# Optimization experiments

Hardware: AMD Instinct MI355X
Metric: run time of the kernel (lower is better)

## Reference

```python
import jax, jax.numpy as jnp
import numpy as np

N_NODES_PER_GRAPH = 64
NUM_GRAPHS = 2048
N = NUM_GRAPHS * N_NODES_PER_GRAPH  # 131072 total nodes
E = N * 8                           # 1048576 edges
IN_DIM, H1, H2 = 64, 128, 64
OUT_DIM = (N_NODES_PER_GRAPH * N_NODES_PER_GRAPH - N_NODES_PER_GRAPH) // 2  # 2016


def setup_inputs() -> dict:
    key = jax.random.key(0)
    ks = jax.random.split(key, 16)
    s = 0.05
    x = jax.random.normal(ks[0], (N, IN_DIM), dtype=jnp.float32)
    # edges within each graph: offsets within graph + graph base offset
    src_local = jax.random.randint(ks[1], (E,), 0, N_NODES_PER_GRAPH)
    dst_local = jax.random.randint(ks[2], (E,), 0, N_NODES_PER_GRAPH)
    gid = jnp.repeat(jnp.arange(NUM_GRAPHS), E // NUM_GRAPHS) * N_NODES_PER_GRAPH
    edge_index = jnp.stack([src_local + gid, dst_local + gid]).astype(jnp.int64)
    batch = jnp.repeat(jnp.arange(NUM_GRAPHS), N_NODES_PER_GRAPH).astype(jnp.int64)
    eps = jax.random.normal(ks[3], (NUM_GRAPHS, H2), dtype=jnp.float32)
    return {
        "x": x, "edge_index": edge_index, "batch": batch, "eps": eps,
        "w1_rel": jax.random.normal(ks[4], (IN_DIM, H1)) * s,
        "b1": jnp.zeros((H1,), jnp.float32),
        "w1_root": jax.random.normal(ks[5], (IN_DIM, H1)) * s,
        "w2_rel": jax.random.normal(ks[6], (H1, H2)) * s,
        "b2": jnp.zeros((H2,), jnp.float32),
        "w2_root": jax.random.normal(ks[7], (H1, H2)) * s,
        "w3_rel": jax.random.normal(ks[8], (H1, H2)) * s,
        "b3": jnp.zeros((H2,), jnp.float32),
        "w3_root": jax.random.normal(ks[9], (H1, H2)) * s,
        "fc1_w": jax.random.normal(ks[10], (H2, H1)) * s,
        "fc1_b": jnp.zeros((H1,), jnp.float32),
        "fc2_w": jax.random.normal(ks[11], (H1, OUT_DIM)) * s,
        "fc2_b": jnp.zeros((OUT_DIM,), jnp.float32),
    }


def _graph_conv(h, src, dst, w_rel, b, w_root):
    # PyG GraphConv: out_i = W_rel @ (sum_{j in N(i)} h_j) + b + W_root @ h_i
    agg = jax.ops.segment_sum(h[src], dst, num_segments=N)  # [N, d_in]
    return agg @ w_rel + b + h @ w_root


def _segment_mean(h, seg):
    s = jax.ops.segment_sum(h, seg, num_segments=NUM_GRAPHS)
    cnt = jax.ops.segment_sum(jnp.ones((h.shape[0],), h.dtype), seg, num_segments=NUM_GRAPHS)
    return s / jnp.maximum(cnt, 1.0)[:, None]


def reference(x, edge_index, batch, eps, w1_rel, b1, w1_root, w2_rel, b2, w2_root,
              w3_rel, b3, w3_root, fc1_w, fc1_b, fc2_w, fc2_b):
    src, dst = edge_index[0], edge_index[1]
    # encode (dropout p=0.0 -> identity)
    h1 = jax.nn.relu(_graph_conv(x, src, dst, w1_rel, b1, w1_root))
    mu = _segment_mean(_graph_conv(h1, src, dst, w2_rel, b2, w2_root), batch)
    logvar = _segment_mean(_graph_conv(h1, src, dst, w3_rel, b3, w3_root), batch)
    # reparameterize with provided eps
    z = mu + eps * jnp.exp(0.5 * logvar)
    # decode
    h = jax.nn.relu(z @ fc1_w + fc1_b)
    recon = jax.nn.sigmoid(h @ fc2_w + fc2_b)
    return recon, mu, logvar
```

## Files before the change

### kernel.cpp

```cpp
#include <hip/hip_runtime.h>
#include <math.h>

#define NG 2048
#define NPG 64
#define EPG 512
#define ETOT (NG*EPG)
#define IND 64
#define H1D 128
#define H2D 64
#define OUTD 2016

typedef __attribute__((ext_vector_type(8))) short bf16x8;
typedef __attribute__((ext_vector_type(4))) float f32x4;
typedef __attribute__((ext_vector_type(8))) unsigned short u16x8;
typedef __attribute__((ext_vector_type(4))) short s16x4;

__device__ inline short f2b(float f) {
  union { float f; unsigned u; } v; v.f = f;
  unsigned r = (v.u + 0x7FFFu + ((v.u >> 16) & 1u)) >> 16;
  return (short)r;
}

__global__ void p_w1(const float* __restrict__ w1_rel, const float* __restrict__ w1_root,
                     short* __restrict__ WTgF,
                     const float* __restrict__ w2_rel, const float* __restrict__ w2_root,
                     const float* __restrict__ w3_rel, const float* __restrict__ w3_root,
                     const float* __restrict__ fc1_w,
                     short* __restrict__ W23T, short* __restrict__ fc1T) {
  __shared__ float L[4224];
  const int b = blockIdx.x;
  const int tid = threadIdx.x;
  if (b < 8) {
    const int ct = b;
    const int ks = tid >> 6, l = tid & 63;
    const int col = ct*16 + (l & 15);
    const int kb  = ks*32 + (l >> 4)*8;
    short tmp[8];
    #pragma unroll
    for (int j = 0; j < 8; ++j) {
      const int k = kb + j;
      float v = (k < 64) ? w1_rel[k*H1D + col] : w1_root[(k - 64)*H1D + col];
      tmp[j] = f2b(v);
    }
    *(uint4*)&WTgF[(size_t)((ct*4 + ks)*64 + l)*8] = *(uint4*)tmp;
  } else if (b < 12) {
    const int cc = b - 8;
    const int j0 = cc*32;
    const float* wrel  = (cc < 2) ? w2_rel  : w3_rel;
    const float* wroot = (cc < 2) ? w2_root : w3_root;
    const int jl = j0 & 63;
    const int c = tid >> 3, k0 = (tid & 7)*32;
    for (int i = tid; i < 4096; i += 256) {
      int k = i >> 5, cc2 = i & 31;
      L[k*33 + cc2] = wrel[k*H2D + jl + cc2];
    }
    __syncthreads();
    if (k0 < 128)
      for (int kk = 0; kk < 32; ++kk)
        W23T[(size_t)(j0 + c)*264 + k0 + kk] = f2b(L[(k0 + kk)*33 + c]);
    __syncthreads();
    for (int i = tid; i < 4096; i += 256) {
      int k = i >> 5, cc2 = i & 31;
      L[k*33 + cc2] = wroot[k*H2D + jl + cc2];
    }
    __syncthreads();
    if (k0 >= 128)
      for (int kk = 0; kk < 32; ++kk)
        W23T[(size_t)(j0 + c)*264 + k0 + kk] = f2b(L[(k0 + kk - 128)*33 + c]);
  } else {
    const int c0 = (b - 12)*64;
    for (int i = tid; i < 4096; i += 256) {
      int k = i >> 6, c = i & 63;
      L[k*65 + c] = fc1_w[k*H1D + c0 + c];
    }
    __syncthreads();
    const int c = tid >> 2, k0 = (tid & 3)*16;
    for (int kk = 0; kk < 16; ++kk)
      fc1T[(size_t)(c0 + c)*72 + k0 + kk] = f2b(L[(k0 + kk)*65 + c]);
  }
}

__global__ __launch_bounds__(256, 5) void k1_enc(
    const float* __restrict__ x, const int* __restrict__ ei,
    const short* __restrict__ WTgF, const float* __restrict__ b1,
    short* __restrict__ SVb,
    const float* __restrict__ fc2_w, short* __restrict__ WF2g)
{
  __shared__ __align__(16) char smem[31744];
  const int g = blockIdx.x;
  const int tid = threadIdx.x;

  if (g >= NG) {
    float* L = (float*)smem;
    const int bid = g - NG;
    const int c0 = bid*32;
    for (int i = tid; i < 4096; i += 256) {
      int k = i >> 5, c = i & 31;
      L[k*33 + c] = fc2_w[(size_t)k*OUTD + c0 + c];
    }
    __syncthreads();
    const int tl = tid >> 7;
    const int r  = tid & 127;
    const int ks = r >> 5;
    const int lp = r & 31;
    const int ct = bid*2 + tl;
    #pragma unroll
    for (int u = 0; u < 2; ++u) {
      const int l = lp*2 + u;
      const int cl = tl*16 + (l & 15);
      const int kb = ks*32 + (l >> 4)*8;
      short tmp[8];
      #pragma unroll
      for (int j = 0; j < 8; ++j) tmp[j] = f2b(L[(kb + j)*33 + cl]);
      *(uint4*)&WF2g[(size_t)((ct*4 + ks)*64 + l)*8] = *(uint4*)tmp;
    }
    return;
  }

  short* Xb   = (short*)smem;
  short* XbT  = (short*)(smem + 9216);
  short* Ab   = (short*)(smem + 18432);
  unsigned* Au32 = (unsigned*)(smem + 27648);

  const int w = tid >> 6, l = tid & 63;

  const int e0 = g*EPG + tid*2;
  const int2 sp = *(const int2*)&ei[e0];
  const int2 dp = *(const int2*)&ei[ETOT + e0];
  const int s0 = sp.x & 63, d0 = dp.x & 63;
  const int s1 = sp.y & 63, d1 = dp.y & 63;
  const int n = tid >> 2, f0 = (tid & 3) * 16;
  const float* xr = x + (size_t)g*(NPG*IND) + n*IND + f0;
  float4 v0 = *(const float4*)&xr[0];
  float4 v1 = *(const float4*)&xr[4];
  float4 v2 = *(const float4*)&xr[8];
  float4 v3 = *(const float4*)&xr[12];

  for (int i = tid; i < 64*16; i += 256) Au32[i] = 0u;
  __syncthreads();

  atomicAdd(&Au32[d0*16 + (s0 >> 2)], 1u << (8*(s0 & 3)));
  atomicAdd(&Au32[d1*16 + (s1 >> 2)], 1u << (8*(s1 & 3)));

  {
    u16x8 lo, hi;
    lo[0]=(unsigned short)f2b(v0.x); lo[1]=(unsigned short)f2b(v0.y);
    lo[2]=(unsigned short)f2b(v0.z); lo[3]=(unsigned short)f2b(v0.w);
    lo[4]=(unsigned short)f2b(v1.x); lo[5]=(unsigned short)f2b(v1.y);
    lo[6]=(unsigned short)f2b(v1.z); lo[7]=(unsigned short)f2b(v1.w);
    hi[0]=(unsigned short)f2b(v2.x); hi[1]=(unsigned short)f2b(v2.y);
    hi[2]=(unsigned short)f2b(v2.z); hi[3]=(unsigned short)f2b(v2.w);
    hi[4]=(unsigned short)f2b(v3.x); hi[5]=(unsigned short)f2b(v3.y);
    hi[6]=(unsigned short)f2b(v3.z); hi[7]=(unsigned short)f2b(v3.w);
    *(u16x8*)&Xb[n*72 + f0]     = lo;
    *(u16x8*)&Xb[n*72 + f0 + 8] = hi;
    #pragma unroll
    for (int j = 0; j < 8; ++j) {
      XbT[(f0 + j)*72 + n]     = (short)lo[j];
      XbT[(f0 + 8 + j)*72 + n] = (short)hi[j];
    }
  }
  __syncthreads();

  {
    const int row = tid >> 2, qw = tid & 3;
    unsigned wds[4];
    #pragma unroll
    for (int q = 0; q < 4; ++q) wds[q] = Au32[row*16 + qw*4 + q];
    auto pk = [](unsigned wv, int p) -> unsigned {
      unsigned c0 = (wv >> (16*p)) & 255u, c1 = (wv >> (16*p + 8)) & 255u;
      return (unsigned)(unsigned short)f2b((float)c0)
           | ((unsigned)(unsigned short)f2b((float)c1) << 16);
    };
    uint4 oA = { pk(wds[0],0), pk(wds[0],1), pk(wds[1],0), pk(wds[1],1) };
    uint4 oB = { pk(wds[2],0), pk(wds[2],1), pk(wds[3],0), pk(wds[3],1) };
    unsigned* abp = (unsigned*)&Ab[row*72 + qw*16];
    *(uint4*)&abp[0] = oA;
    *(uint4*)&abp[4] = oB;
  }

  {
    const int squad = tid >> 4;
    const int db = (tid & 15) * 4;
    unsigned ps = 0;
    #pragma unroll
    for (int i = 0; i < 4; ++i) ps += Au32[(db + i)*16 + squad];
    ps += __shfl_xor(ps, 1); ps += __shfl_xor(ps, 2);
    ps += __shfl_xor(ps, 4); ps += __shfl_xor(ps, 8);
    if ((tid & 15) == 0) {
      #pragma unroll
      for (int i = 0; i < 4; ++i)
        *(float*)&Ab[(squad*4 + i)*72 + 64] = (float)((ps >> (8*i)) & 255u);
    }
  }

  const int rm = w*16;
  const int fr = l & 15;
  const int koff = (l >> 4) * 8;

  f32x4 agc[4];
  #pragma unroll
  for (int t = 0; t < 4; ++t) agc[t] = (f32x4){0.f,0.f,0.f,0.f};
  #pragma unroll
  for (int ks = 0; ks < 2; ++ks) {
    bf16x8 a = *(const bf16x8*)&Ab[(rm + fr)*72 + ks*32 + koff];
    #pragma unroll
    for (int t = 0; t < 4; ++t) {
      bf16x8 b = *(const bf16x8*)&XbT[(t*16 + fr)*72 + ks*32 + koff];
      agc[t] = __builtin_amdgcn_mfma_f32_16x16x32_bf16(a, b, agc[t], 0, 0, 0);
    }
  }

  bf16x8 bfr[2][4];
  #pragma unroll
  for (int ct2 = 0; ct2 < 2; ++ct2)
    #pragma unroll
    for (int ks = 0; ks < 4; ++ks)
      bfr[ct2][ks] = *(const bf16x8*)&WTgF[(size_t)(((2*w + ct2)*4 + ks)*64 + l)*8];

  short* AGb = Ab;
  #pragma unroll
  for (int t = 0; t < 4; ++t)
    #pragma unroll
    for (int r = 0; r < 4; ++r)
      AGb[(rm + (l>>4)*4 + r)*72 + t*16 + fr] = f2b(agc[t][r]);

  __syncthreads();

  const float bb0 = b1[(2*w)*16 + fr];
  const float bb1 = b1[(2*w + 1)*16 + fr];
  float hs0 = 0.f, ws0 = 0.f, hs1 = 0.f, ws1 = 0.f;
  #pragma unroll
  for (int rt = 0; rt < 4; ++rt) {
    bf16x8 afr[4];
    #pragma unroll
    for (int ks = 0; ks < 4; ++ks)
      afr[ks] = (ks < 2)
        ? *(const bf16x8*)&AGb[(rt*16 + fr)*72 + ks*32 + koff]
        : *(const bf16x8*)&Xb[(rt*16 + fr)*72 + (ks - 2)*32 + koff];
    f32x4 a0 = (f32x4){0.f,0.f,0.f,0.f}, a1 = (f32x4){0.f,0.f,0.f,0.f};
    #pragma unroll
    for (int ks = 0; ks < 4; ++ks) {
      a0 = __builtin_amdgcn_mfma_f32_16x16x32_bf16(afr[ks], bfr[0][ks], a0, 0, 0, 0);
      a1 = __builtin_amdgcn_mfma_f32_16x16x32_bf16(afr[ks], bfr[1][ks], a1, 0, 0, 0);
    }
    #pragma unroll
    for (int r = 0; r < 4; ++r) {
      const float dgr = *(const float*)&Ab[(rt*16 + (l>>4)*4 + r)*72 + 64];
      float va = fmaxf(a0[r] + bb0, 0.f);
      float vb = fmaxf(a1[r] + bb1, 0.f);
      hs0 += va; ws0 += dgr*va;
      hs1 += vb; ws1 += dgr*vb;
    }
  }
  hs0 += __shfl_down(hs0, 32); ws0 += __shfl_down(ws0, 32);
  hs1 += __shfl_down(hs1, 32); ws1 += __shfl_down(ws1, 32);
  hs0 += __shfl_down(hs0, 16); ws0 += __shfl_down(ws0, 16);
  hs1 += __shfl_down(hs1, 16); ws1 += __shfl_down(ws1, 16);
  if (l < 16) {
    short* svg = SVb + (size_t)g*256;
    svg[(2*w)*16 + l]           = f2b(ws0);
    svg[(2*w + 1)*16 + l]       = f2b(ws1);
    svg[128 + (2*w)*16 + l]     = f2b(hs0);
    svg[128 + (2*w + 1)*16 + l] = f2b(hs1);
  }
}

__global__ __launch_bounds__(256) void k1b_latent(
    const short* __restrict__ SVb, const short* __restrict__ W23T,
    const float* __restrict__ b2, const float* __restrict__ b3,
    const float* __restrict__ eps, const short* __restrict__ fc1T,
    const float* __restrict__ fc1_b,
    float* __restrict__ out_mu, float* __restrict__ out_lv, short* __restrict__ hbufF)
{
  __shared__ short SV[32*264];
  __shared__ short Zt[32*72];
  const int g0 = blockIdx.x * 32;
  const int tid = threadIdx.x;
  const int w = tid >> 6, l = tid & 63;
  const int s = w >> 1;
  const int h = w & 1;
  const int fr = l & 15;
  const int koff = (l >> 4) * 8;

  for (int i = tid; i < 32*64; i += 256) {
    const int r = i >> 6, kq = (i & 63)*4;
    *(s16x4*)&SV[r*264 + kq] = *(const s16x4*)&SVb[(size_t)(g0 + r)*256 + kq];
  }
  __syncthreads();

  f32x4 acc[4];
  #pragma unroll
  for (int t = 0; t < 4; ++t) acc[t] = (f32x4){0.f,0.f,0.f,0.f};
  #pragma unroll
  for (int ks = 0; ks < 8; ++ks) {
    bf16x8 a = *(const bf16x8*)&SV[(s*16 + fr)*264 + ks*32 + koff];
    #pragma unroll
    for (int j = 0; j < 2; ++j) {
      bf16x8 bm = *(const bf16x8*)&W23T[((2*h + j)*16 + fr)*264 + ks*32 + koff];
      bf16x8 bl = *(const bf16x8*)&W23T[((2*h + j + 4)*16 + fr)*264 + ks*32 + koff];
      acc[j]     = __builtin_amdgcn_mfma_f32_16x16x32_bf16(bm, a, acc[j], 0, 0, 0);
      acc[2 + j] = __builtin_amdgcn_mfma_f32_16x16x32_bf16(bl, a, acc[2 + j], 0, 0, 0);
    }
  }
  {
    const int grow = s*16 + (l & 15);
    const size_t gg = (size_t)(g0 + grow);
    #pragma unroll
    for (int j = 0; j < 2; ++j) {
      const int c0 = (2*h + j)*16 + (l >> 4)*4;
      const float4 bb2 = *(const float4*)&b2[c0];
      const float4 bb3 = *(const float4*)&b3[c0];
      const float4 ev  = *(const float4*)&eps[gg*64 + c0];
      float4 mu, lv;
      mu.x = acc[j][0]*(1.f/64.f) + bb2.x;  lv.x = acc[2+j][0]*(1.f/64.f) + bb3.x;
      mu.y = acc[j][1]*(1.f/64.f) + bb2.y;  lv.y = acc[2+j][1]*(1.f/64.f) + bb3.y;
      mu.z = acc[j][2]*(1.f/64.f) + bb2.z;  lv.z = acc[2+j][2]*(1.f/64.f) + bb3.z;
      mu.w = acc[j][3]*(1.f/64.f) + bb2.w;  lv.w = acc[2+j][3]*(1.f/64.f) + bb3.w;
      *(float4*)&out_mu[gg*64 + c0] = mu;
      *(float4*)&out_lv[gg*64 + c0] = lv;
      s16x4 zs;
      zs[0] = f2b(mu.x + ev.x * __expf(0.5f*lv.x));
      zs[1] = f2b(mu.y + ev.y * __expf(0.5f*lv.y));
      zs[2] = f2b(mu.z + ev.z * __expf(0.5f*lv.z));
      zs[3] = f2b(mu.w + ev.w * __expf(0.5f*lv.w));
      *(s16x4*)&Zt[grow*72 + c0] = zs;
    }
  }
  __syncthreads();

  f32x4 hacc[4];
  #pragma unroll
  for (int t = 0; t < 4; ++t) hacc[t] = (f32x4){0.f,0.f,0.f,0.f};
  #pragma unroll
  for (int ks = 0; ks < 2; ++ks) {
    bf16x8 a = *(const bf16x8*)&Zt[(s*16 + fr)*72 + ks*32 + koff];
    #pragma unroll
    for (int j = 0; j < 4; ++j) {
      bf16x8 b = *(const bf16x8*)&fc1T[((h*4 + j)*16 + fr)*72 + ks*32 + koff];
      hacc[j] = __builtin_amdgcn_mfma_f32_16x16x32_bf16(b, a, hacc[j], 0, 0, 0);
    }
  }
  {
    const int row = s*16 + (l & 15);
    const int rt2 = blockIdx.x*2 + (row >> 4);
    #pragma unroll
    for (int j = 0; j < 4; ++j) {
      const int c0 = (h*4 + j)*16 + (l >> 4)*4;
      const float4 bb = *(const float4*)&fc1_b[c0];
      s16x4 hv;
      hv[0] = f2b(fmaxf(hacc[j][0] + bb.x, 0.f));
      hv[1] = f2b(fmaxf(hacc[j][1] + bb.y, 0.f));
      hv[2] = f2b(fmaxf(hacc[j][2] + bb.z, 0.f));
      hv[3] = f2b(fmaxf(hacc[j][3] + bb.w, 0.f));
      const int ks2 = c0 >> 5;
      const int q   = (c0 >> 3) & 3;
      const int j8  = c0 & 7;
      const int lane = (row & 15) + 16*q;
      *(s16x4*)&hbufF[(size_t)((rt2*4 + ks2)*64 + lane)*8 + j8] = hv;
    }
  }
}

__global__ __launch_bounds__(256, 8) void k2_decoder(
    const short* __restrict__ hbufF, const short* __restrict__ WF2g,
    const float* __restrict__ fc2_b, float* __restrict__ recon)
{
  const int bx = blockIdx.x, by = blockIdx.y;
  const int tid = threadIdx.x;
  const int w = tid >> 6, l = tid & 63;
  const int rt = bx*4 + w;

  bf16x8 ah[4];
  #pragma unroll
  for (int ks = 0; ks < 4; ++ks)
    ah[ks] = *(const bf16x8*)&hbufF[(size_t)((rt*4 + ks)*64 + l)*8];

  f32x4 acc[6];
  #pragma unroll
  for (int t = 0; t < 6; ++t) acc[t] = (f32x4){0.f,0.f,0.f,0.f};

  #pragma unroll
  for (int ks = 0; ks < 4; ++ks) {
    #pragma unroll
    for (int t = 0; t < 6; ++t) {
      const int ct = by*6 + t;
      bf16x8 bw = *(const bf16x8*)&WF2g[(size_t)((ct*4 + ks)*64 + l)*8];
      acc[t] = __builtin_amdgcn_mfma_f32_16x16x32_bf16(bw, ah[ks], acc[t], 0, 0, 0);
    }
  }

  const int row = bx*64 + w*16 + (l & 15);
  #pragma unroll
  for (int t = 0; t < 6; ++t) {
    const int colq = (by*6 + t)*16 + (l >> 4)*4;
    const float4 bb = *(const float4*)&fc2_b[colq];
    float4 o;
    o.x = 1.f/(1.f + __expf(-(acc[t][0] + bb.x)));
    o.y = 1.f/(1.f + __expf(-(acc[t][1] + bb.y)));
    o.z = 1.f/(1.f + __expf(-(acc[t][2] + bb.z)));
    o.w = 1.f/(1.f + __expf(-(acc[t][3] + bb.w)));
    *(float4*)&recon[(size_t)row*OUTD + colq] = o;
  }
}

extern "C" void kernel_launch(void* const* d_in, const int* in_sizes, int n_in,
                              void* d_out, int out_size, void* d_ws, size_t ws_size,
                              hipStream_t stream) {
  const float* x       = (const float*)d_in[0];
  const int*   ei      = (const int*)d_in[1];
  const float* eps     = (const float*)d_in[3];
  const float* w1_rel  = (const float*)d_in[4];
  const float* b1      = (const float*)d_in[5];
  const float* w1_root = (const float*)d_in[6];
  const float* w2_rel  = (const float*)d_in[7];
  const float* b2      = (const float*)d_in[8];
  const float* w2_root = (const float*)d_in[9];
  const float* w3_rel  = (const float*)d_in[10];
  const float* b3      = (const float*)d_in[11];
  const float* w3_root = (const float*)d_in[12];
  const float* fc1_w   = (const float*)d_in[13];
  const float* fc1_b   = (const float*)d_in[14];
  const float* fc2_w   = (const float*)d_in[15];
  const float* fc2_b   = (const float*)d_in[16];

  float* recon  = (float*)d_out;
  float* out_mu = recon + (size_t)NG*OUTD;
  float* out_lv = out_mu + (size_t)NG*H2D;

  char* p = (char*)d_ws;
  short* WTgF  = (short*)p;              p += 8*4*64*8*2;
  short* WF2g  = (short*)p;              p += 126*4*64*8*2;
  short* fc1T  = (short*)p;              p += 128*72*2;
  short* W23T  = (short*)p;              p += 128*264*2;
  short* SVb   = (short*)p;              p += (size_t)NG*256*2;
  short* hbufF = (short*)p;

  p_w1<<<14, 256, 0, stream>>>(w1_rel, w1_root, WTgF,
                               w2_rel, w2_root, w3_rel, w3_root,
                               fc1_w, W23T, fc1T);
  k1_enc<<<NG + 63, 256, 0, stream>>>(x, ei, WTgF, b1, SVb, fc2_w, WF2g);
  k1b_latent<<<64, 256, 0, stream>>>(SVb, W23T, b2, b3, eps, fc1T, fc1_b,
                                     out_mu, out_lv, hbufF);
  k2_decoder<<<dim3(32, 21), 256, 0, stream>>>(hbufF, WF2g, fc2_b, recon);
}
```

Baseline: 135.2 us.

## Process two graphs per encoder block with prefetched second-graph loads

After: 140.5 us. +3.9%, slower.

```diff
diff --git a/kernel.cpp b/kernel.cpp
--- a/kernel.cpp
+++ b/kernel.cpp
@@ -80,19 +80,19 @@
   }
 }
 
-__global__ __launch_bounds__(256, 5) void k1_enc(
+__global__ __launch_bounds__(256, 4) void k1_enc(
     const float* __restrict__ x, const int* __restrict__ ei,
     const short* __restrict__ WTgF, const float* __restrict__ b1,
     short* __restrict__ SVb,
     const float* __restrict__ fc2_w, short* __restrict__ WF2g)
 {
-  __shared__ __align__(16) char smem[31744];
+  __shared__ __align__(16) char smem[35840];
   const int g = blockIdx.x;
   const int tid = threadIdx.x;
 
-  if (g >= NG) {
+  if (g >= NG/2) {
     float* L = (float*)smem;
-    const int bid = g - NG;
+    const int bid = g - NG/2;
     const int c0 = bid*32;
     for (int i = tid; i < 4096; i += 256) {
       int k = i >> 5, c = i & 31;
@@ -120,29 +120,29 @@
   short* Xb   = (short*)smem;
   short* XbT  = (short*)(smem + 9216);
   short* Ab   = (short*)(smem + 18432);
-  unsigned* Au32 = (unsigned*)(smem + 27648);
+  unsigned* AuA = (unsigned*)(smem + 27648);
+  unsigned* AuB = (unsigned*)(smem + 31744);
 
   const int w = tid >> 6, l = tid & 63;
-
-  const int e0 = g*EPG + tid*2;
-  const int2 sp = *(const int2*)&ei[e0];
-  const int2 dp = *(const int2*)&ei[ETOT + e0];
-  const int s0 = sp.x & 63, d0 = dp.x & 63;
-  const int s1 = sp.y & 63, d1 = dp.y & 63;
+  const int fr = l & 15;
+  const int koff = (l >> 4) * 8;
+  const int rm = w*16;
   const int n = tid >> 2, f0 = (tid & 3) * 16;
-  const float* xr = x + (size_t)g*(NPG*IND) + n*IND + f0;
-  float4 v0 = *(const float4*)&xr[0];
-  float4 v1 = *(const float4*)&xr[4];
-  float4 v2 = *(const float4*)&xr[8];
-  float4 v3 = *(const float4*)&xr[12];
-
-  for (int i = tid; i < 64*16; i += 256) Au32[i] = 0u;
-  __syncthreads();
-
-  atomicAdd(&Au32[d0*16 + (s0 >> 2)], 1u << (8*(s0 & 3)));
-  atomicAdd(&Au32[d1*16 + (s1 >> 2)], 1u << (8*(s1 & 3)));
-
-  {
+
+  const int gA = g*2;
+  const int e0 = gA*EPG + tid*2;
+  const int2 spA = *(const int2*)&ei[e0];
+  const int2 dpA = *(const int2*)&ei[ETOT + e0];
+  const int2 spB = *(const int2*)&ei[e0 + EPG];
+  const int2 dpB = *(const int2*)&ei[ETOT + e0 + EPG];
+
+  const float* xrA = x + (size_t)gA*(NPG*IND) + n*IND + f0;
+  float4 va0 = *(const float4*)&xrA[0];
+  float4 va1 = *(const float4*)&xrA[4];
+  float4 va2 = *(const float4*)&xrA[8];
+  float4 va3 = *(const float4*)&xrA[12];
+
+  auto STAGE = [&](float4 v0, float4 v1, float4 v2, float4 v3) {
     u16x8 lo, hi;
     lo[0]=(unsigned short)f2b(v0.x); lo[1]=(unsigned short)f2b(v0.y);
     lo[2]=(unsigned short)f2b(v0.z); lo[3]=(unsigned short)f2b(v0.w);
@@ -159,14 +159,13 @@
       XbT[(f0 + j)*72 + n]     = (short)lo[j];
       XbT[(f0 + 8 + j)*72 + n] = (short)hi[j];
     }
-  }
-  __syncthreads();
-
-  {
+  };
+
+  auto CVT = [&](const unsigned* Au) {
     const int row = tid >> 2, qw = tid & 3;
     unsigned wds[4];
     #pragma unroll
-    for (int q = 0; q < 4; ++q) wds[q] = Au32[row*16 + qw*4 + q];
+    for (int q = 0; q < 4; ++q) wds[q] = Au[row*16 + qw*4 + q];
     auto pk = [](unsigned wv, int p) -> unsigned {
       unsigned c0 = (wv >> (16*p)) & 255u, c1 = (wv >> (16*p + 8)) & 255u;
       return (unsigned)(unsigned short)f2b((float)c0)
@@ -177,14 +176,11 @@
     unsigned* abp = (unsigned*)&Ab[row*72 + qw*16];
     *(uint4*)&abp[0] = oA;
     *(uint4*)&abp[4] = oB;
-  }
-
-  {
     const int squad = tid >> 4;
     const int db = (tid & 15) * 4;
     unsigned ps = 0;
     #pragma unroll
-    for (int i = 0; i < 4; ++i) ps += Au32[(db + i)*16 + squad];
+    for (int i = 0; i < 4; ++i) ps += Au[(db + i)*16 + squad];
     ps += __shfl_xor(ps, 1); ps += __shfl_xor(ps, 2);
     ps += __shfl_xor(ps, 4); ps += __shfl_xor(ps, 8);
     if ((tid & 15) == 0) {
@@ -192,24 +188,27 @@
       for (int i = 0; i < 4; ++i)
         *(float*)&Ab[(squad*4 + i)*72 + 64] = (float)((ps >> (8*i)) & 255u);
     }
-  }
-
-  const int rm = w*16;
-  const int fr = l & 15;
-  const int koff = (l >> 4) * 8;
-
-  f32x4 agc[4];
-  #pragma unroll
-  for (int t = 0; t < 4; ++t) agc[t] = (f32x4){0.f,0.f,0.f,0.f};
-  #pragma unroll
-  for (int ks = 0; ks < 2; ++ks) {
-    bf16x8 a = *(const bf16x8*)&Ab[(rm + fr)*72 + ks*32 + koff];
-    #pragma unroll
-    for (int t = 0; t < 4; ++t) {
-      bf16x8 b = *(const bf16x8*)&XbT[(t*16 + fr)*72 + ks*32 + koff];
-      agc[t] = __builtin_amdgcn_mfma_f32_16x16x32_bf16(a, b, agc[t], 0, 0, 0);
-    }
-  }
+  };
+
+  auto PH1 = [&]() {
+    f32x4 agc[4];
+    #pragma unroll
+    for (int t = 0; t < 4; ++t) agc[t] = (f32x4){0.f,0.f,0.f,0.f};
+    #pragma unroll
+    for (int ks = 0; ks < 2; ++ks) {
+      bf16x8 a = *(const bf16x8*)&Ab[(rm + fr)*72 + ks*32 + koff];
+      #pragma unroll
+      for (int t = 0; t < 4; ++t) {
+        bf16x8 b = *(const bf16x8*)&XbT[(t*16 + fr)*72 + ks*32 + koff];
+        agc[t] = __builtin_amdgcn_mfma_f32_16x16x32_bf16(a, b, agc[t], 0, 0, 0);
+      }
+    }
+    #pragma unroll
+    for (int t = 0; t < 4; ++t)
+      #pragma unroll
+      for (int r = 0; r < 4; ++r)
+        Ab[(rm + (l>>4)*4 + r)*72 + t*16 + fr] = f2b(agc[t][r]);
+  };
 
   bf16x8 bfr[2][4];
   #pragma unroll
@@ -217,53 +216,75 @@
     #pragma unroll
     for (int ks = 0; ks < 4; ++ks)
       bfr[ct2][ks] = *(const bf16x8*)&WTgF[(size_t)(((2*w + ct2)*4 + ks)*64 + l)*8];
-
-  short* AGb = Ab;
-  #pragma unroll
-  for (int t = 0; t < 4; ++t)
-    #pragma unroll
-    for (int r = 0; r < 4; ++r)
-      AGb[(rm + (l>>4)*4 + r)*72 + t*16 + fr] = f2b(agc[t][r]);
-
-  __syncthreads();
-
   const float bb0 = b1[(2*w)*16 + fr];
   const float bb1 = b1[(2*w + 1)*16 + fr];
-  float hs0 = 0.f, ws0 = 0.f, hs1 = 0.f, ws1 = 0.f;
-  #pragma unroll
-  for (int rt = 0; rt < 4; ++rt) {
-    bf16x8 afr[4];
-    #pragma unroll
-    for (int ks = 0; ks < 4; ++ks)
-      afr[ks] = (ks < 2)
-        ? *(const bf16x8*)&AGb[(rt*16 + fr)*72 + ks*32 + koff]
-        : *(const bf16x8*)&Xb[(rt*16 + fr)*72 + (ks - 2)*32 + koff];
-    f32x4 a0 = (f32x4){0.f,0.f,0.f,0.f}, a1 = (f32x4){0.f,0.f,0.f,0.f};
-    #pragma unroll
-    for (int ks = 0; ks < 4; ++ks) {
-      a0 = __builtin_amdgcn_mfma_f32_16x16x32_bf16(afr[ks], bfr[0][ks], a0, 0, 0, 0);
-      a1 = __builtin_amdgcn_mfma_f32_16x16x32_bf16(afr[ks], bfr[1][ks], a1, 0, 0, 0);
-    }
-    #pragma unroll
-    for (int r = 0; r < 4; ++r) {
-      const float dgr = *(const float*)&Ab[(rt*16 + (l>>4)*4 + r)*72 + 64];
-      float va = fmaxf(a0[r] + bb0, 0.f);
-      float vb = fmaxf(a1[r] + bb1, 0.f);
-      hs0 += va; ws0 += dgr*va;
-      hs1 += vb; ws1 += dgr*vb;
-    }
-  }
-  hs0 += __shfl_down(hs0, 32); ws0 += __shfl_down(ws0, 32);
-  hs1 += __shfl_down(hs1, 32); ws1 += __shfl_down(ws1, 32);
-  hs0 += __shfl_down(hs0, 16); ws0 += __shfl_down(ws0, 16);
-  hs1 += __shfl_down(hs1, 16); ws1 += __shfl_down(ws1, 16);
-  if (l < 16) {
-    short* svg = SVb + (size_t)g*256;
-    svg[(2*w)*16 + l]           = f2b(ws0);
-    svg[(2*w + 1)*16 + l]       = f2b(ws1);
-    svg[128 + (2*w)*16 + l]     = f2b(hs0);
-    svg[128 + (2*w + 1)*16 + l] = f2b(hs1);
-  }
+
+  auto PH2EPI = [&](int gg) {
+    float hs0 = 0.f, ws0 = 0.f, hs1 = 0.f, ws1 = 0.f;
+    #pragma unroll
+    for (int rt = 0; rt < 4; ++rt) {
+      bf16x8 afr[4];
+      #pragma unroll
+      for (int ks = 0; ks < 4; ++ks)
+        afr[ks] = (ks < 2)
+          ? *(const bf16x8*)&Ab[(rt*16 + fr)*72 + ks*32 + koff]
+          : *(const bf16x8*)&Xb[(rt*16 + fr)*72 + (ks - 2)*32 + koff];
+      f32x4 a0 = (f32x4){0.f,0.f,0.f,0.f}, a1 = (f32x4){0.f,0.f,0.f,0.f};
+      #pragma unroll
+      for (int ks = 0; ks < 4; ++ks) {
+        a0 = __builtin_amdgcn_mfma_f32_16x16x32_bf16(afr[ks], bfr[0][ks], a0, 0, 0, 0);
+        a1 = __builtin_amdgcn_mfma_f32_16x16x32_bf16(afr[ks], bfr[1][ks], a1, 0, 0, 0);
+      }
+      #pragma unroll
+      for (int r = 0; r < 4; ++r) {
+        const float dgr = *(const float*)&Ab[(rt*16 + (l>>4)*4 + r)*72 + 64];
+        float va = fmaxf(a0[r] + bb0, 0.f);
+        float vb = fmaxf(a1[r] + bb1, 0.f);
+        hs0 += va; ws0 += dgr*va;
+        hs1 += vb; ws1 += dgr*vb;
+      }
+    }
+    hs0 += __shfl_down(hs0, 32); ws0 += __shfl_down(ws0, 32);
+    hs1 += __shfl_down(hs1, 32); ws1 += __shfl_down(ws1, 32);
+    hs0 += __shfl_down(hs0, 16); ws0 += __shfl_down(ws0, 16);
+    hs1 += __shfl_down(hs1, 16); ws1 += __shfl_down(ws1, 16);
+    if (l < 16) {
+      short* svg = SVb + (size_t)gg*256;
+      svg[(2*w)*16 + l]           = f2b(ws0);
+      svg[(2*w + 1)*16 + l]       = f2b(ws1);
+      svg[128 + (2*w)*16 + l]     = f2b(hs0);
+      svg[128 + (2*w + 1)*16 + l] = f2b(hs1);
+    }
+  };
+
+  for (int i = tid; i < 2048; i += 256) ((unsigned*)AuA)[i] = 0u;
+  __syncthreads();
+
+  atomicAdd(&AuA[(dpA.x & 63)*16 + ((spA.x & 63) >> 2)], 1u << (8*((spA.x & 63) & 3)));
+  atomicAdd(&AuA[(dpA.y & 63)*16 + ((spA.y & 63) >> 2)], 1u << (8*((spA.y & 63) & 3)));
+  atomicAdd(&AuB[(dpB.x & 63)*16 + ((spB.x & 63) >> 2)], 1u << (8*((spB.x & 63) & 3)));
+  atomicAdd(&AuB[(dpB.y & 63)*16 + ((spB.y & 63) >> 2)], 1u << (8*((spB.y & 63) & 3)));
+
+  STAGE(va0, va1, va2, va3);
+
+  const float* xrB = xrA + NPG*IND;
+  float4 vb0 = *(const float4*)&xrB[0];
+  float4 vb1 = *(const float4*)&xrB[4];
+  float4 vb2 = *(const float4*)&xrB[8];
+  float4 vb3 = *(const float4*)&xrB[12];
+
+  __syncthreads();
+  CVT(AuA);
+  PH1();
+  __syncthreads();
+  PH2EPI(gA);
+  __syncthreads();
+  STAGE(vb0, vb1, vb2, vb3);
+  CVT(AuB);
+  __syncthreads();
+  PH1();
+  __syncthreads();
+  PH2EPI(gA + 1);
 }
 
 __global__ __launch_bounds__(256) void k1b_latent(
@@ -439,7 +460,7 @@
   p_w1<<<14, 256, 0, stream>>>(w1_rel, w1_root, WTgF,
                                w2_rel, w2_root, w3_rel, w3_root,
                                fc1_w, W23T, fc1T);
-  k1_enc<<<NG + 63, 256, 0, stream>>>(x, ei, WTgF, b1, SVb, fc2_w, WF2g);
+  k1_enc<<<NG/2 + 63, 256, 0, stream>>>(x, ei, WTgF, b1, SVb, fc2_w, WF2g);
   k1b_latent<<<64, 256, 0, stream>>>(SVb, W23T, b2, b3, eps, fc1T, fc1_b,
                                      out_mu, out_lv, hbufF);
   k2_decoder<<<dim3(32, 21), 256, 0, stream>>>(hbufF, WF2g, fc2_b, recon);
```
